# Performance work log

Measured on AMD Instinct MI355X. Metric: run time of the kernel, lower is better.

The kernel has to match this reference:

```python
import jax, jax.numpy as jnp
import numpy as np

B, N, E, H = 8, 2000, 20, 128


def setup_inputs() -> dict:
    key = jax.random.key(0)
    ks = jax.random.split(key, 9)
    s = 1.0 / np.sqrt(H)
    return {
        "x": jax.random.normal(ks[0], (B, N, H), dtype=jnp.float32),
        "e": jax.random.normal(ks[1], (B, N * E, H), dtype=jnp.float32),
        "Wu": jax.random.uniform(ks[2], (H, H), jnp.float32, -s, s),
        "bu": jax.random.uniform(ks[3], (H,), jnp.float32, -s, s),
        "Wv": jax.random.uniform(ks[4], (H, H), jnp.float32, -s, s),
        "bv": jax.random.uniform(ks[5], (H,), jnp.float32, -s, s),
        "We": jax.random.uniform(ks[6], (H, H), jnp.float32, -s, s),
        "be": jax.random.uniform(ks[7], (H,), jnp.float32, -s, s),
        "edge_index": jax.random.randint(ks[8], (B, N * E), 0, N, dtype=jnp.int32),
        "n_edges": E,
    }


def reference(x, e, Wu, bu, Wv, bv, We, be, edge_index, n_edges):
    b, n, h = x.shape
    Ux = x @ Wu + bu                      # [B, N, H] node self-embedding
    Vx = x @ Wv + bv                      # [B, N, H] neighbor embedding
    Ve = e @ We + be                      # [B, N*E, H] edge embedding
    # softmax over the n_edges axis per (node, channel)
    Ve = jax.nn.softmax(Ve.reshape(b, n, n_edges, h), axis=2)
    # gather neighbor features along node axis via edge_index
    Vx_g = jnp.take_along_axis(Vx, edge_index[..., None], axis=1)  # [B, N*E, H]
    to = (Ve * Vx_g.reshape(b, n, n_edges, h)).sum(axis=2)          # [B, N, H]
    return Ux + to
```

## Files before the change

### kernel.cpp

```cpp
#include <hip/hip_runtime.h>

#define B_   8
#define NN   2000
#define EE   20
#define HH   128
#define BN   (B_*NN)
#define NE   (NN*EE)

typedef unsigned short ushort_t;
typedef __bf16 bf16x8 __attribute__((ext_vector_type(8)));
typedef float  f32x4  __attribute__((ext_vector_type(4)));
typedef float  f4     __attribute__((ext_vector_type(4)));
typedef unsigned short us8 __attribute__((ext_vector_type(8)));
typedef unsigned short us4 __attribute__((ext_vector_type(4)));

union FragU { us8 u; bf16x8 b; };
union Frag32 { unsigned int w[4]; us8 u; bf16x8 b; };

__device__ __forceinline__ float b2f(ushort_t v) {
    union { unsigned int i; float f; } c; c.i = ((unsigned int)v) << 16; return c.f;
}
__device__ __forceinline__ ushort_t f2b(float f) {
    union { float f; unsigned int i; } c; c.f = f;
    unsigned int r = (c.i + 0x7FFFu + ((c.i >> 16) & 1u)) >> 16;
    return (ushort_t)r;
}

__global__ __launch_bounds__(256) void k1_embed(
    const float* __restrict__ x,
    const float* __restrict__ Wu, const float* __restrict__ bu,
    const float* __restrict__ Wv, const float* __restrict__ bv,
    ushort_t* __restrict__ Uxb, ushort_t* __restrict__ Vxb)
{
    const int tid  = threadIdx.x;
    const int lane = tid & 63;
    const int wave = tid >> 6;
    const int wm = wave >> 1, wn = wave & 1;
    const int q  = lane >> 4, ln = lane & 15;
    const int m0 = blockIdx.x * 64;
    const int sel = blockIdx.y;
    const float* W    = sel ? Wv : Wu;
    const float* bias = sel ? bv : bu;
    ushort_t* dst = sel ? Vxb : Uxb;

    FragU af[2][4];
#pragma unroll
    for (int tm = 0; tm < 2; ++tm)
#pragma unroll
        for (int ki = 0; ki < 4; ++ki) {
            const float* p = x + (size_t)(m0 + wm * 32 + tm * 16 + ln) * HH + ki * 32 + q * 8;
            f4 lo = *(const f4*)(p);
            f4 hi = *(const f4*)(p + 4);
            us8 t;
#pragma unroll
            for (int r = 0; r < 4; ++r) { t[r] = f2b(lo[r]); t[r + 4] = f2b(hi[r]); }
            af[tm][ki].u = t;
        }

    FragU bf[4][4];
#pragma unroll
    for (int ki = 0; ki < 4; ++ki)
#pragma unroll
        for (int tn = 0; tn < 4; ++tn) {
            int n = wn * 64 + tn * 16 + ln;
            us8 t;
#pragma unroll
            for (int i = 0; i < 8; ++i) t[i] = f2b(W[(ki * 32 + q * 8 + i) * HH + n]);
            bf[ki][tn].u = t;
        }

    f32x4 acc[2][4];
#pragma unroll
    for (int tm = 0; tm < 2; ++tm)
#pragma unroll
        for (int tn = 0; tn < 4; ++tn) acc[tm][tn] = (f32x4){0.f, 0.f, 0.f, 0.f};

#pragma unroll
    for (int ki = 0; ki < 4; ++ki)
#pragma unroll
        for (int tm = 0; tm < 2; ++tm)
#pragma unroll
            for (int tn = 0; tn < 4; ++tn)
                acc[tm][tn] = __builtin_amdgcn_mfma_f32_16x16x32_bf16(
                    af[tm][ki].b, bf[ki][tn].b, acc[tm][tn], 0, 0, 0);

#pragma unroll
    for (int tn = 0; tn < 4; ++tn) {
        int col = wn * 64 + tn * 16 + ln;
        float bb = bias[col];
#pragma unroll
        for (int tm = 0; tm < 2; ++tm) {
            int rowb = m0 + wm * 32 + tm * 16 + q * 4;
#pragma unroll
            for (int r = 0; r < 4; ++r)
                dst[(size_t)(rowb + r) * HH + col] = f2b(acc[tm][tn][r] + bb);
        }
    }
}

#define CSTR 84

__global__ __launch_bounds__(256, 3) void k2_fused(
    const float* __restrict__ e, const float* __restrict__ We,
    const int* __restrict__ eidx,
    const ushort_t* __restrict__ Uxb, const ushort_t* __restrict__ Vxb,
    float* __restrict__ out)
{
    __shared__ __align__(16) ushort_t CT[128 * CSTR];
    __shared__ int sidx[80];

    const int tid  = threadIdx.x;
    const int lane = tid & 63;
    const int wave = tid >> 6;
    const int q  = lane >> 4, ln = lane & 15;

    const int b   = blockIdx.y;
    const int nl0 = blockIdx.x * 4;
    const size_t erow0 = (size_t)b * NE + (size_t)nl0 * EE;

    if (tid < 80) sidx[tid] = eidx[erow0 + tid];

    FragU bfr[4][2];
#pragma unroll
    for (int ki = 0; ki < 4; ++ki)
#pragma unroll
        for (int tn = 0; tn < 2; ++tn) {
            int n = wave * 32 + tn * 16 + ln;
            us8 t;
#pragma unroll
            for (int i = 0; i < 8; ++i) t[i] = f2b(We[(ki * 32 + q * 8 + i) * HH + n]);
            bfr[ki][tn].u = t;
        }

    f32x4 acc[5][2];
#pragma unroll
    for (int tm = 0; tm < 5; ++tm)
#pragma unroll
        for (int tn = 0; tn < 2; ++tn) acc[tm][tn] = (f32x4){0.f, 0.f, 0.f, 0.f};

    const float* ap = e + (erow0 + ln) * (size_t)HH + q * 8;
#pragma unroll
    for (int ki = 0; ki < 4; ++ki) {
        Frag32 af[5];
#pragma unroll
        for (int tm = 0; tm < 5; ++tm) {
            const float* p = ap + tm * 16 * HH + ki * 32;
            f4 lo = *(const f4*)(p);
            f4 hi = *(const f4*)(p + 4);
            asm("v_cvt_pk_bf16_f32 %0, %1, %2" : "=v"(af[tm].w[0]) : "v"(lo[0]), "v"(lo[1]));
            asm("v_cvt_pk_bf16_f32 %0, %1, %2" : "=v"(af[tm].w[1]) : "v"(lo[2]), "v"(lo[3]));
            asm("v_cvt_pk_bf16_f32 %0, %1, %2" : "=v"(af[tm].w[2]) : "v"(hi[0]), "v"(hi[1]));
            asm("v_cvt_pk_bf16_f32 %0, %1, %2" : "=v"(af[tm].w[3]) : "v"(hi[2]), "v"(hi[3]));
        }
#pragma unroll
        for (int tm = 0; tm < 5; ++tm)
#pragma unroll
            for (int tn = 0; tn < 2; ++tn)
                acc[tm][tn] = __builtin_amdgcn_mfma_f32_16x16x32_bf16(
                    af[tm].b, bfr[ki][tn].b, acc[tm][tn], 0, 0, 0);
    }

#pragma unroll
    for (int tm = 0; tm < 5; ++tm)
#pragma unroll
        for (int tn = 0; tn < 2; ++tn) {
            int col  = wave * 32 + tn * 16 + ln;
            int rowb = tm * 16 + q * 4;
            us4 pk;
#pragma unroll
            for (int r = 0; r < 4; ++r) pk[r] = f2b(acc[tm][tn][r]);
            *(us4*)(&CT[col * CSTR + rowb]) = pk;
        }

    __syncthreads();

    const int h  = tid & 127;
    const int gp = tid >> 7;
#pragma unroll 1
    for (int j = 0; j < 2; ++j) {
        int g = gp + 2 * j;
        const ushort_t* ctp = &CT[h * CSTR + g * 20];
        float lv[20];
#pragma unroll
        for (int i = 0; i < 5; ++i) {
            us4 v = *(const us4*)(ctp + i * 4);
#pragma unroll
            for (int r = 0; r < 4; ++r) lv[i * 4 + r] = b2f(v[r]);
        }
        float mx = lv[0];
#pragma unroll
        for (int k = 1; k < EE; ++k) mx = fmaxf(mx, lv[k]);

        ushort_t gv[20];
        const int ib = g * 20;
#pragma unroll
        for (int k = 0; k < EE; ++k)
            gv[k] = Vxb[(size_t)(b * NN + sidx[ib + k]) * HH + h];

        float s = 0.f, a = 0.f;
#pragma unroll
        for (int k = 0; k < EE; ++k) {
            float p = __expf(lv[k] - mx);
            s += p;
            a = fmaf(p, b2f(gv[k]), a);
        }
        size_t orow = (size_t)(b * NN + nl0 + g) * HH + h;
        out[orow] = b2f(Uxb[orow]) + a / s;
    }
}

extern "C" void kernel_launch(void* const* d_in, const int* in_sizes, int n_in,
                              void* d_out, int out_size, void* d_ws, size_t ws_size,
                              hipStream_t stream) {
    const float* x  = (const float*)d_in[0];
    const float* e  = (const float*)d_in[1];
    const float* Wu = (const float*)d_in[2];
    const float* bu = (const float*)d_in[3];
    const float* Wv = (const float*)d_in[4];
    const float* bv = (const float*)d_in[5];
    const float* We = (const float*)d_in[6];
    const int*   eidx = (const int*)d_in[8];

    ushort_t* Uxb = (ushort_t*)d_ws;
    ushort_t* Vxb = (ushort_t*)((char*)d_ws + (size_t)BN * HH * 2);
    float*    o   = (float*)d_out;

    k1_embed<<<dim3(250, 2), 256, 0, stream>>>(x, Wu, bu, Wv, bv, Uxb, Vxb);
    k2_fused<<<dim3(500, 8), 256, 0, stream>>>(e, We, eidx, Uxb, Vxb, o);
}
```

Baseline: 315.9 us.

## Split fused edge kernel into separate logits GEMM and softmax-gather epilogue

Breaks the fused edge-embedding plus softmax kernel into two kernels. The first is a plain GEMM that writes bf16 edge logits to workspace, with We prescaled by log2(e). The second reads those logits, applies exp2 without max subtraction, gathers Vx, and normalizes with a fast reciprocal. The aim is to drop the LDS transpose, the barrier and the max reduction, and to let each kernel run at its own occupancy. In exchange it adds a bf16 logits round trip through global memory, about 82 MB each way, and relies on the logits being small enough that skipping max subtraction cannot overflow.

```diff
diff --git a/kernel.cpp b/kernel.cpp
--- a/kernel.cpp
+++ b/kernel.cpp
@@ -6,6 +6,7 @@
 #define HH   128
 #define BN   (B_*NN)
 #define NE   (NN*EE)
+#define TOTE (B_*NE)
 
 typedef unsigned short ushort_t;
 typedef __bf16 bf16x8 __attribute__((ext_vector_type(8)));
@@ -13,9 +14,9 @@
 typedef float  f4     __attribute__((ext_vector_type(4)));
 typedef unsigned short us8 __attribute__((ext_vector_type(8)));
 typedef unsigned short us4 __attribute__((ext_vector_type(4)));
+typedef int    i4     __attribute__((ext_vector_type(4)));
 
 union FragU { us8 u; bf16x8 b; };
-union Frag32 { unsigned int w[4]; us8 u; bf16x8 b; };
 
 __device__ __forceinline__ float b2f(ushort_t v) {
     union { unsigned int i; float f; } c; c.i = ((unsigned int)v) << 16; return c.f;
@@ -98,114 +99,115 @@
     }
 }
 
-#define CSTR 84
-
-__global__ __launch_bounds__(256, 3) void k2_fused(
+__global__ __launch_bounds__(256) void k2a_logits(
     const float* __restrict__ e, const float* __restrict__ We,
-    const int* __restrict__ eidx,
+    ushort_t* __restrict__ Ve)
+{
+    const int tid  = threadIdx.x;
+    const int lane = tid & 63;
+    const int wave = tid >> 6;
+    const int wm = wave >> 1, wn = wave & 1;
+    const int q  = lane >> 4, ln = lane & 15;
+    const int m0 = blockIdx.x * 64;
+
+    FragU af[2][4];
+#pragma unroll
+    for (int tm = 0; tm < 2; ++tm)
+#pragma unroll
+        for (int ki = 0; ki < 4; ++ki) {
+            const float* p = e + (size_t)(m0 + wm * 32 + tm * 16 + ln) * HH + ki * 32 + q * 8;
+            f4 lo = *(const f4*)(p);
+            f4 hi = *(const f4*)(p + 4);
+            us8 t;
+#pragma unroll
+            for (int r = 0; r < 4; ++r) { t[r] = f2b(lo[r]); t[r + 4] = f2b(hi[r]); }
+            af[tm][ki].u = t;
+        }
+
+    FragU bf[4][4];
+#pragma unroll
+    for (int ki = 0; ki < 4; ++ki)
+#pragma unroll
+        for (int tn = 0; tn < 4; ++tn) {
+            int n = wn * 64 + tn * 16 + ln;
+            us8 t;
+#pragma unroll
+            for (int i = 0; i < 8; ++i)
+                t[i] = f2b(We[(ki * 32 + q * 8 + i) * HH + n] * 1.44269504089f);
+            bf[ki][tn].u = t;
+        }
+
+    f32x4 acc[2][4];
+#pragma unroll
+    for (int tm = 0; tm < 2; ++tm)
+#pragma unroll
+        for (int tn = 0; tn < 4; ++tn) acc[tm][tn] = (f32x4){0.f, 0.f, 0.f, 0.f};
+
+#pragma unroll
+    for (int ki = 0; ki < 4; ++ki)
+#pragma unroll
+        for (int tm = 0; tm < 2; ++tm)
+#pragma unroll
+            for (int tn = 0; tn < 4; ++tn)
+                acc[tm][tn] = __builtin_amdgcn_mfma_f32_16x16x32_bf16(
+                    af[tm][ki].b, bf[ki][tn].b, acc[tm][tn], 0, 0, 0);
+
+#pragma unroll
+    for (int tn = 0; tn < 4; ++tn) {
+        int col = wn * 64 + tn * 16 + ln;
+#pragma unroll
+        for (int tm = 0; tm < 2; ++tm) {
+            int rowb = m0 + wm * 32 + tm * 16 + q * 4;
+#pragma unroll
+            for (int r = 0; r < 4; ++r)
+                Ve[(size_t)(rowb + r) * HH + col] = f2b(acc[tm][tn][r]);
+        }
+    }
+}
+
+__global__ __launch_bounds__(256) void k2b_epilogue(
+    const ushort_t* __restrict__ Ve, const int* __restrict__ eidx,
     const ushort_t* __restrict__ Uxb, const ushort_t* __restrict__ Vxb,
     float* __restrict__ out)
 {
-    __shared__ __align__(16) ushort_t CT[128 * CSTR];
-    __shared__ int sidx[80];
-
-    const int tid  = threadIdx.x;
-    const int lane = tid & 63;
-    const int wave = tid >> 6;
-    const int q  = lane >> 4, ln = lane & 15;
-
-    const int b   = blockIdx.y;
-    const int nl0 = blockIdx.x * 4;
-    const size_t erow0 = (size_t)b * NE + (size_t)nl0 * EE;
-
-    if (tid < 80) sidx[tid] = eidx[erow0 + tid];
-
-    FragU bfr[4][2];
-#pragma unroll
-    for (int ki = 0; ki < 4; ++ki)
-#pragma unroll
-        for (int tn = 0; tn < 2; ++tn) {
-            int n = wave * 32 + tn * 16 + ln;
-            us8 t;
-#pragma unroll
-            for (int i = 0; i < 8; ++i) t[i] = f2b(We[(ki * 32 + q * 8 + i) * HH + n]);
-            bfr[ki][tn].u = t;
-        }
-
-    f32x4 acc[5][2];
-#pragma unroll
-    for (int tm = 0; tm < 5; ++tm)
-#pragma unroll
-        for (int tn = 0; tn < 2; ++tn) acc[tm][tn] = (f32x4){0.f, 0.f, 0.f, 0.f};
-
-    const float* ap = e + (erow0 + ln) * (size_t)HH + q * 8;
-#pragma unroll
-    for (int ki = 0; ki < 4; ++ki) {
-        Frag32 af[5];
-#pragma unroll
-        for (int tm = 0; tm < 5; ++tm) {
-            const float* p = ap + tm * 16 * HH + ki * 32;
-            f4 lo = *(const f4*)(p);
-            f4 hi = *(const f4*)(p + 4);
-            asm("v_cvt_pk_bf16_f32 %0, %1, %2" : "=v"(af[tm].w[0]) : "v"(lo[0]), "v"(lo[1]));
-            asm("v_cvt_pk_bf16_f32 %0, %1, %2" : "=v"(af[tm].w[1]) : "v"(lo[2]), "v"(lo[3]));
-            asm("v_cvt_pk_bf16_f32 %0, %1, %2" : "=v"(af[tm].w[2]) : "v"(hi[0]), "v"(hi[1]));
-            asm("v_cvt_pk_bf16_f32 %0, %1, %2" : "=v"(af[tm].w[3]) : "v"(hi[2]), "v"(hi[3]));
-        }
-#pragma unroll
-        for (int tm = 0; tm < 5; ++tm)
-#pragma unroll
-            for (int tn = 0; tn < 2; ++tn)
-                acc[tm][tn] = __builtin_amdgcn_mfma_f32_16x16x32_bf16(
-                    af[tm].b, bfr[ki][tn].b, acc[tm][tn], 0, 0, 0);
-    }
-
-#pragma unroll
-    for (int tm = 0; tm < 5; ++tm)
-#pragma unroll
-        for (int tn = 0; tn < 2; ++tn) {
-            int col  = wave * 32 + tn * 16 + ln;
-            int rowb = tm * 16 + q * 4;
-            us4 pk;
-#pragma unroll
-            for (int r = 0; r < 4; ++r) pk[r] = f2b(acc[tm][tn][r]);
-            *(us4*)(&CT[col * CSTR + rowb]) = pk;
-        }
-
-    __syncthreads();
-
-    const int h  = tid & 127;
-    const int gp = tid >> 7;
+    const int tid = threadIdx.x;
+    const int h   = tid & 127;
+    const int np  = tid >> 7;
+    const int n0  = blockIdx.x * 16;
+
 #pragma unroll 1
-    for (int j = 0; j < 2; ++j) {
-        int g = gp + 2 * j;
-        const ushort_t* ctp = &CT[h * CSTR + g * 20];
-        float lv[20];
-#pragma unroll
-        for (int i = 0; i < 5; ++i) {
-            us4 v = *(const us4*)(ctp + i * 4);
-#pragma unroll
-            for (int r = 0; r < 4; ++r) lv[i * 4 + r] = b2f(v[r]);
-        }
-        float mx = lv[0];
-#pragma unroll
-        for (int k = 1; k < EE; ++k) mx = fmaxf(mx, lv[k]);
-
+    for (int j = 0; j < 8; ++j) {
+        const int gnode = n0 + np + 2 * j;
+        const int bb    = gnode / NN;
+        const size_t er = (size_t)gnode * EE;
+
+        i4 iv[5];
+#pragma unroll
+        for (int i = 0; i < 5; ++i) iv[i] = *(const i4*)(eidx + er + 4 * i);
+
+        const ushort_t* vp = Ve + er * HH + h;
+        ushort_t lz[20];
+#pragma unroll
+        for (int k = 0; k < EE; ++k) lz[k] = vp[(size_t)k * HH];
+
+        const ushort_t* vb = Vxb + (size_t)bb * NN * HH + h;
         ushort_t gv[20];
-        const int ib = g * 20;
-#pragma unroll
-        for (int k = 0; k < EE; ++k)
-            gv[k] = Vxb[(size_t)(b * NN + sidx[ib + k]) * HH + h];
+#pragma unroll
+        for (int i = 0; i < 5; ++i)
+#pragma unroll
+            for (int r = 0; r < 4; ++r)
+                gv[i * 4 + r] = vb[(size_t)iv[i][r] * HH];
+
+        const ushort_t ux = Uxb[(size_t)gnode * HH + h];
 
         float s = 0.f, a = 0.f;
 #pragma unroll
         for (int k = 0; k < EE; ++k) {
-            float p = __expf(lv[k] - mx);
+            float p = exp2f(b2f(lz[k]));
             s += p;
             a = fmaf(p, b2f(gv[k]), a);
         }
-        size_t orow = (size_t)(b * NN + nl0 + g) * HH + h;
-        out[orow] = b2f(Uxb[orow]) + a / s;
+        out[(size_t)gnode * HH + h] = b2f(ux) + a * __builtin_amdgcn_rcpf(s);
     }
 }
 
@@ -223,8 +225,10 @@
 
     ushort_t* Uxb = (ushort_t*)d_ws;
     ushort_t* Vxb = (ushort_t*)((char*)d_ws + (size_t)BN * HH * 2);
+    ushort_t* Ve  = (ushort_t*)((char*)d_ws + (size_t)2 * BN * HH * 2);
     float*    o   = (float*)d_out;
 
-    k1_embed<<<dim3(250, 2), 256, 0, stream>>>(x, Wu, bu, Wv, bv, Uxb, Vxb);
-    k2_fused<<<dim3(500, 8), 256, 0, stream>>>(e, We, eidx, Uxb, Vxb, o);
-}
+    k1_embed  <<<dim3(250, 2), 256, 0, stream>>>(x, Wu, bu, Wv, bv, Uxb, Vxb);
+    k2a_logits<<<dim3(TOTE / 64), 256, 0, stream>>>(e, We, Ve);
+    k2b_epilogue<<<dim3(BN / 16), 256, 0, stream>>>(Ve, eidx, Uxb, Vxb, o);
+}
```

Measured after the change: 332.5 us. +5.3%, slower.
